# Kernel tuning notes

Measured on AMD Instinct MI355X. Metric: run time of the kernel, lower is better.

The kernel has to match this reference:

```python
import jax, jax.numpy as jnp
import numpy as np

N, K, F, E = 50000, 32, 128, 8

def setup_inputs() -> dict:
    key = jax.random.key(0)
    k1, k2, k3, k4, k5 = jax.random.split(key, 5)
    nodes = jax.random.normal(k1, (N, F), dtype=jnp.float32)
    nlist = jax.random.randint(k2, (N, K), 0, N, dtype=jnp.int64)
    edges = jax.random.normal(k3, (N, K, E), dtype=jnp.float32)
    inv_degree = jax.random.uniform(k4, (N,), dtype=jnp.float32)
    w = jax.random.normal(k5, (F, F, E), dtype=jnp.float32)
    return {"nodes": nodes, "nlist": nlist, "edges": edges,
            "inv_degree": inv_degree, "w": w}

def reference(nodes, nlist, edges, inv_degree, w):
    # gather neighbor features: [N, K, F]
    sliced = nodes[nlist]
    # 3-way contraction with neighbor-sum and inverse-degree scaling
    # edges: ijn (N,K,E); sliced: ijl (N,K,F); w: lmn (F,F,E); inv_degree: i
    out = jnp.einsum('ijn,ijl,lmn,i->im', edges, sliced, w, inv_degree)
    # activation is None (linear) per init_kwargs
    return out
```

## Files before the change

kernel.cpp:

```cpp
#include <hip/hip_runtime.h>
#include <hip/hip_bf16.h>

static constexpr int NN  = 50000;
static constexpr int KNB = 32;
static constexpr int F   = 128;
static constexpr int E   = 8;
static constexpr int TI  = 16;
static constexpr int LN  = F * E;

typedef __attribute__((ext_vector_type(8))) short short8v;
typedef __attribute__((ext_vector_type(4))) float f32x4;

__device__ __forceinline__ unsigned short f2bf(float x) {
    unsigned u = __float_as_uint(x);
    unsigned r = (u + 0x7fff + ((u >> 16) & 1)) >> 16;
    return (unsigned short)r;
}
__device__ __forceinline__ float bf2f(unsigned short b) {
    return __uint_as_float(((unsigned)b) << 16);
}

__global__ void prep_w_kernel(const float* __restrict__ w, unsigned short* __restrict__ w2f) {
    int o  = blockIdx.x * 256 + threadIdx.x;
    int e8 = o & 7, kq = (o >> 3) & 3, m = (o >> 5) & 127, kb = o >> 12;
    int k  = kb * 32 + kq * 4 + (e8 & 3) + ((e8 >> 2) << 4);
    int l  = k >> 3, n = k & 7;
    w2f[o] = f2bf(w[(size_t)(l * F + m) * E + n]);
}

__global__ void prep_nodes_kernel(const float* __restrict__ nodes, unsigned short* __restrict__ nb) {
    int t = blockIdx.x * 256 + threadIdx.x;
    const float4* s = (const float4*)nodes + (size_t)t * 2;
    float4 a = s[0], b = s[1];
    uint4 pk;
    pk.x = (unsigned)f2bf(a.x) | ((unsigned)f2bf(a.y) << 16);
    pk.y = (unsigned)f2bf(a.z) | ((unsigned)f2bf(a.w) << 16);
    pk.z = (unsigned)f2bf(b.x) | ((unsigned)f2bf(b.y) << 16);
    pk.w = (unsigned)f2bf(b.z) | ((unsigned)f2bf(b.w) << 16);
    ((uint4*)nb)[t] = pk;
}

template<bool NB>
__global__ __launch_bounds__(512, 8)
void mp_main_kernel(const float* __restrict__ nodes,
                    const unsigned short* __restrict__ nodesBf,
                    const int*   __restrict__ nlist,
                    const float* __restrict__ edges,
                    const float* __restrict__ inv_degree,
                    const unsigned short* __restrict__ w2f,
                    float* __restrict__ out)
{
    __shared__ unsigned short tS[TI * LN];
    const int tid    = threadIdx.x;
    const int wv     = __builtin_amdgcn_readfirstlane(tid >> 6);
    const int lane   = tid & 63;
    const int i_base = blockIdx.x * TI;
    char* tB = (char*)tS;

    for (int it = 0; it < 2; ++it) {
        const int row = wv * 2 + it;
        const int i   = i_base + row;
        const int*   nl = nlist + (size_t)i * KNB;
        const float* ep = edges + (size_t)i * (KNB * E);

        unsigned g[KNB];
        if (NB) {
            #pragma unroll
            for (int j = 0; j < KNB; ++j) {
                unsigned idx = (unsigned)nl[j];
                if (idx >= (unsigned)NN) idx = 0u;
                g[j] = ((const unsigned*)(nodesBf + (size_t)idx * F))[lane];
            }
        } else {
            #pragma unroll
            for (int j = 0; j < KNB; ++j) {
                unsigned idx = (unsigned)nl[j];
                if (idx >= (unsigned)NN) idx = 0u;
                const float2 fv = ((const float2*)(nodes + (size_t)idx * F))[lane];
                g[j] = ((unsigned)f2bf(fv.y) << 16) | (unsigned)f2bf(fv.x);
            }
        }
        __builtin_amdgcn_sched_barrier(0);

        float a0[E], a1[E];
        #pragma unroll
        for (int n = 0; n < E; ++n) { a0[n] = 0.f; a1[n] = 0.f; }
        #pragma unroll
        for (int j = 0; j < KNB; ++j) {
            const float v0 = bf2f((unsigned short)(g[j] & 0xffff));
            const float v1 = bf2f((unsigned short)(g[j] >> 16));
            const float4 e0 = *(const float4*)(ep + j * 8);
            const float4 e1 = *(const float4*)(ep + j * 8 + 4);
            a0[0] = __builtin_fmaf(e0.x, v0, a0[0]); a1[0] = __builtin_fmaf(e0.x, v1, a1[0]);
            a0[1] = __builtin_fmaf(e0.y, v0, a0[1]); a1[1] = __builtin_fmaf(e0.y, v1, a1[1]);
            a0[2] = __builtin_fmaf(e0.z, v0, a0[2]); a1[2] = __builtin_fmaf(e0.z, v1, a1[2]);
            a0[3] = __builtin_fmaf(e0.w, v0, a0[3]); a1[3] = __builtin_fmaf(e0.w, v1, a1[3]);
            a0[4] = __builtin_fmaf(e1.x, v0, a0[4]); a1[4] = __builtin_fmaf(e1.x, v1, a1[4]);
            a0[5] = __builtin_fmaf(e1.y, v0, a0[5]); a1[5] = __builtin_fmaf(e1.y, v1, a1[5]);
            a0[6] = __builtin_fmaf(e1.z, v0, a0[6]); a1[6] = __builtin_fmaf(e1.z, v1, a1[6]);
            a0[7] = __builtin_fmaf(e1.w, v0, a0[7]); a1[7] = __builtin_fmaf(e1.w, v1, a1[7]);
        }

        uint4 pk0, pk1;
        pk0.x = (unsigned)f2bf(a0[0]) | ((unsigned)f2bf(a0[1]) << 16);
        pk0.y = (unsigned)f2bf(a0[2]) | ((unsigned)f2bf(a0[3]) << 16);
        pk0.z = (unsigned)f2bf(a0[4]) | ((unsigned)f2bf(a0[5]) << 16);
        pk0.w = (unsigned)f2bf(a0[6]) | ((unsigned)f2bf(a0[7]) << 16);
        pk1.x = (unsigned)f2bf(a1[0]) | ((unsigned)f2bf(a1[1]) << 16);
        pk1.y = (unsigned)f2bf(a1[2]) | ((unsigned)f2bf(a1[3]) << 16);
        pk1.z = (unsigned)f2bf(a1[4]) | ((unsigned)f2bf(a1[5]) << 16);
        pk1.w = (unsigned)f2bf(a1[6]) | ((unsigned)f2bf(a1[7]) << 16);
        const int p2 = (lane >> 2) & 1;
        const int s  = (row & 7) << 4;
        const int rb = row * (LN * 2);
        const uint4 first  = p2 ? pk1 : pk0;
        const uint4 second = p2 ? pk0 : pk1;
        *(uint4*)(tB + rb + ((lane * 32 + (p2 << 4))      ^ s)) = first;
        *(uint4*)(tB + rb + ((lane * 32 + 16 - (p2 << 4)) ^ s)) = second;
    }
    __syncthreads();

    const int colm = lane & 15;
    const int kq   = lane >> 4;
    const int mt   = wv;

    f32x4 c0 = {0.f, 0.f, 0.f, 0.f};

    const int arow = colm * (LN * 2);
    const int asw  = (colm & 7) << 4;

    #pragma unroll 4
    for (int kb = 0; kb < LN / 32; ++kb) {
        union { short8v v; uint2 u[2]; } af;
        af.u[0] = *(const uint2*)(tB + arow + ((kb * 64      + kq * 8) ^ asw));
        af.u[1] = *(const uint2*)(tB + arow + ((kb * 64 + 32 + kq * 8) ^ asw));
        union { short8v v; uint4 u; } b0;
        b0.u = *(const uint4*)(w2f + ((size_t)((kb * 128 + mt * 16 + colm) * 4 + kq)) * 8);
        c0 = __builtin_amdgcn_mfma_f32_16x16x32_bf16(af.v, b0.v, c0, 0, 0, 0);
    }

    #pragma unroll
    for (int r = 0; r < 4; ++r) {
        const int ii = kq * 4 + r;
        const int gi = i_base + ii;
        out[(size_t)gi * F + mt * 16 + colm] = inv_degree[gi] * c0[r];
    }
}

__global__ __launch_bounds__(256, 2)
void mp_fused_fallback(const float* __restrict__ nodes, const int* __restrict__ nlist,
                       const float* __restrict__ edges, const float* __restrict__ inv_degree,
                       const float* __restrict__ w, float* __restrict__ out)
{
    __shared__ float tLds[TI * F * E];
    const int tid = threadIdx.x;
    const int i_base = blockIdx.x * TI;
    {
        const int l = tid & (F - 1);
        const int half = __builtin_amdgcn_readfirstlane(tid >> 7);
        for (int g = 0; g < TI / 2; ++g) {
            const int ii = g * 2 + half;
            const int i = i_base + ii;
            float acc[E];
            #pragma unroll
            for (int n = 0; n < E; ++n) acc[n] = 0.f;
            const int* nl = nlist + i * KNB;
            const float* ep = edges + (size_t)i * (KNB * E);
            #pragma unroll 4
            for (int j = 0; j < KNB; ++j) {
                unsigned idx = (unsigned)nl[j];
                if (idx >= (unsigned)NN) idx = 0u;
                const float v = nodes[idx * F + l];
                #pragma unroll
                for (int n = 0; n < E; ++n) acc[n] = __builtin_fmaf(ep[j * E + n], v, acc[n]);
            }
            float4* dst = (float4*)&tLds[ii * (F * E) + l * E];
            dst[0] = make_float4(acc[0], acc[1], acc[2], acc[3]);
            dst[1] = make_float4(acc[4], acc[5], acc[6], acc[7]);
        }
    }
    __syncthreads();
    const int m_lo = tid & 63;
    const int q = __builtin_amdgcn_readfirstlane(tid >> 6);
    float accA[TI], accB[TI];
    #pragma unroll
    for (int ii = 0; ii < TI; ++ii) { accA[ii] = 0.f; accB[ii] = 0.f; }
    for (int lq = 0; lq < F / 4; ++lq) {
        const int l = q * (F / 4) + lq;
        const float4* wp0 = (const float4*)&w[(size_t)l * (F * E) + (size_t)m_lo * E];
        const float4* wp1 = (const float4*)&w[(size_t)l * (F * E) + (size_t)(m_lo + 64) * E];
        const float4 w0a = wp0[0], w0b = wp0[1];
        const float4 w1a = wp1[0], w1b = wp1[1];
        #pragma unroll
        for (int ii = 0; ii < TI; ++ii) {
            const float4* tp = (const float4*)&tLds[ii * (F * E) + l * E];
            const float4 ta = tp[0], tb = tp[1];
            float sA = accA[ii], sB = accB[ii];
            sA = __builtin_fmaf(ta.x, w0a.x, sA); sA = __builtin_fmaf(ta.y, w0a.y, sA);
            sA = __builtin_fmaf(ta.z, w0a.z, sA); sA = __builtin_fmaf(ta.w, w0a.w, sA);
            sA = __builtin_fmaf(tb.x, w0b.x, sA); sA = __builtin_fmaf(tb.y, w0b.y, sA);
            sA = __builtin_fmaf(tb.z, w0b.z, sA); sA = __builtin_fmaf(tb.w, w0b.w, sA);
            sB = __builtin_fmaf(ta.x, w1a.x, sB); sB = __builtin_fmaf(ta.y, w1a.y, sB);
            sB = __builtin_fmaf(ta.z, w1a.z, sB); sB = __builtin_fmaf(ta.w, w1a.w, sB);
            sB = __builtin_fmaf(tb.x, w1b.x, sB); sB = __builtin_fmaf(tb.y, w1b.y, sB);
            sB = __builtin_fmaf(tb.z, w1b.z, sB); sB = __builtin_fmaf(tb.w, w1b.w, sB);
            accA[ii] = sA; accB[ii] = sB;
        }
    }
    __syncthreads();
    float* pLds = tLds;
    #pragma unroll
    for (int ii = 0; ii < TI; ++ii) {
        pLds[q * (TI * F) + ii * F + m_lo] = accA[ii];
        pLds[q * (TI * F) + ii * F + m_lo + 64] = accB[ii];
    }
    __syncthreads();
    #pragma unroll
    for (int r = 0; r < (TI * F) / 256; ++r) {
        const int o = r * 256 + tid;
        const int ii = o >> 7;
        const int m = o & (F - 1);
        const float s = pLds[0 * (TI * F) + ii * F + m] + pLds[1 * (TI * F) + ii * F + m]
                      + pLds[2 * (TI * F) + ii * F + m] + pLds[3 * (TI * F) + ii * F + m];
        const int i = i_base + ii;
        out[(size_t)i * F + m] = inv_degree[i] * s;
    }
}

extern "C" void kernel_launch(void* const* d_in, const int* in_sizes, int n_in,
                              void* d_out, int out_size, void* d_ws, size_t ws_size,
                              hipStream_t stream) {
    const float* nodes      = (const float*)d_in[0];
    const int*   nlist      = (const int*)d_in[1];
    const float* edges      = (const float*)d_in[2];
    const float* inv_degree = (const float*)d_in[3];
    const float* w          = (const float*)d_in[4];
    float* out = (float*)d_out;
    (void)in_sizes; (void)n_in; (void)out_size;

    const size_t need_w2 = (size_t)LN * F * 2;
    const size_t need_nb = (size_t)NN * F * 2;

    if (ws_size < need_w2) {
        mp_fused_fallback<<<dim3(NN / TI), dim3(256), 0, stream>>>(
            nodes, nlist, edges, inv_degree, w, out);
        return;
    }
    unsigned short* w2f = (unsigned short*)d_ws;
    unsigned short* nb  = (unsigned short*)((char*)d_ws + need_w2);

    prep_w_kernel<<<dim3((LN * F) / 256), dim3(256), 0, stream>>>(w, w2f);
    if (ws_size >= need_w2 + need_nb) {
        prep_nodes_kernel<<<dim3(NN * F / 8 / 256), dim3(256), 0, stream>>>(nodes, nb);
        mp_main_kernel<true><<<dim3(NN / TI), dim3(512), 0, stream>>>(
            nodes, nb, nlist, edges, inv_degree, w2f, out);
    } else {
        mp_main_kernel<false><<<dim3(NN / TI), dim3(512), 0, stream>>>(
            nodes, nb, nlist, edges, inv_degree, w2f, out);
    }
}
```

Baseline: 98.80 us.

## Compute neighbor-edge contraction with MFMA using double-buffered LDS staging

The first-stage contraction over neighbors (edges x gathered node features) moves from per-lane scalar FMAs to a 16x16x32 bf16 MFMA per node. Gathered features are transposed into double-buffered LDS and edges are converted to bf16 fragments, so the next node's gather overlaps the current node's MFMA. This adds 16 block-wide barriers per block, more LDS use and a lower occupancy hint. Edges are now rounded to bf16, which adds some precision loss. The fp32 fallback path is reworked to skip the bf16 round-trip on gathered values.

```diff
diff --git a/kernel.cpp b/kernel.cpp
--- a/kernel.cpp
+++ b/kernel.cpp
@@ -41,7 +41,7 @@
 }
 
 template<bool NB>
-__global__ __launch_bounds__(512, 8)
+__global__ __launch_bounds__(512, 6)
 void mp_main_kernel(const float* __restrict__ nodes,
                     const unsigned short* __restrict__ nodesBf,
                     const int*   __restrict__ nlist,
@@ -51,83 +51,122 @@
                     float* __restrict__ out)
 {
     __shared__ unsigned short tS[TI * LN];
+    __shared__ __align__(16) unsigned short ngT[2][128 * 34];
+    __shared__ __align__(16) unsigned short afS[2][512];
     const int tid    = threadIdx.x;
     const int wv     = __builtin_amdgcn_readfirstlane(tid >> 6);
     const int lane   = tid & 63;
+    const int cl     = lane & 15;
+    const int kq     = lane >> 4;
     const int i_base = blockIdx.x * TI;
     char* tB = (char*)tS;
 
-    for (int it = 0; it < 2; ++it) {
-        const int row = wv * 2 + it;
-        const int i   = i_base + row;
-        const int*   nl = nlist + (size_t)i * KNB;
-        const float* ep = edges + (size_t)i * (KNB * E);
-
-        unsigned g[KNB];
-        if (NB) {
+    if (NB) {
+        auto stage = [&](int k) {
+            const int b  = k & 1;
+            const int gi = i_base + k;
+            const int* nl = nlist + (size_t)gi * KNB;
+            unsigned pvs[4];
             #pragma unroll
-            for (int j = 0; j < KNB; ++j) {
-                unsigned idx = (unsigned)nl[j];
+            for (int jj = 0; jj < 4; ++jj) {
+                unsigned idx = (unsigned)nl[wv * 4 + jj];
                 if (idx >= (unsigned)NN) idx = 0u;
-                g[j] = ((const unsigned*)(nodesBf + (size_t)idx * F))[lane];
-            }
-        } else {
+                pvs[jj] = ((const unsigned*)(nodesBf + (size_t)idx * F))[lane];
+            }
             #pragma unroll
+            for (int jj = 0; jj < 4; ++jj) {
+                const int j = wv * 4 + jj;
+                ngT[b][(2 * lane) * 34 + j]     = (unsigned short)pvs[jj];
+                ngT[b][(2 * lane + 1) * 34 + j] = (unsigned short)(pvs[jj] >> 16);
+            }
+            if (wv == (k & 7)) {
+                unsigned fr[4] = {0u, 0u, 0u, 0u};
+                #pragma unroll
+                for (int e = 0; e < 8; ++e) {
+                    const int j = kq * 4 + (e & 3) + ((e >> 2) << 4);
+                    float v = 0.f;
+                    if (cl < 8) v = edges[(size_t)gi * (KNB * E) + j * E + cl];
+                    fr[e >> 1] |= (unsigned)f2bf(v) << ((e & 1) * 16);
+                }
+                *(uint4*)(&afS[b][lane * 8]) = make_uint4(fr[0], fr[1], fr[2], fr[3]);
+            }
+        };
+        auto compute = [&](int k) {
+            const int b = k & 1;
+            union { short8v v; uint4 u; } ea;
+            ea.u = *(const uint4*)(&afS[b][lane * 8]);
+            const char* ngB = (const char*)&ngT[b][0];
+            const int rowb = (wv * 16 + cl) * 68;
+            union { short8v v; unsigned u[4]; } bb;
+            bb.u[0] = *(const unsigned*)(ngB + rowb + kq * 8);
+            bb.u[1] = *(const unsigned*)(ngB + rowb + kq * 8 + 4);
+            bb.u[2] = *(const unsigned*)(ngB + rowb + 32 + kq * 8);
+            bb.u[3] = *(const unsigned*)(ngB + rowb + 32 + kq * 8 + 4);
+            f32x4 d = {0.f, 0.f, 0.f, 0.f};
+            d = __builtin_amdgcn_mfma_f32_16x16x32_bf16(ea.v, bb.v, d, 0, 0, 0);
+            if (kq < 2) {
+                const unsigned d0 = (unsigned)f2bf(d[0]) | ((unsigned)f2bf(d[1]) << 16);
+                const unsigned d1 = (unsigned)f2bf(d[2]) | ((unsigned)f2bf(d[3]) << 16);
+                const int lg = wv * 16 + cl;
+                const int bp = lg * 16 + kq * 8;
+                *(uint2*)(tB + k * (LN * 2) + (bp ^ ((k & 7) << 4))) = make_uint2(d0, d1);
+            }
+        };
+        stage(0);
+        __syncthreads();
+        for (int k = 0; k < TI; ++k) {
+            if (k < TI - 1) stage(k + 1);
+            compute(k);
+            __syncthreads();
+        }
+    } else {
+        for (int it = 0; it < 2; ++it) {
+            const int row = wv * 2 + it;
+            const int i   = i_base + row;
+            const int*   nl = nlist + (size_t)i * KNB;
+            const float* ep = edges + (size_t)i * (KNB * E);
+            float a0[E], a1[E];
+            #pragma unroll
+            for (int n = 0; n < E; ++n) { a0[n] = 0.f; a1[n] = 0.f; }
+            #pragma unroll 4
             for (int j = 0; j < KNB; ++j) {
                 unsigned idx = (unsigned)nl[j];
                 if (idx >= (unsigned)NN) idx = 0u;
                 const float2 fv = ((const float2*)(nodes + (size_t)idx * F))[lane];
-                g[j] = ((unsigned)f2bf(fv.y) << 16) | (unsigned)f2bf(fv.x);
-            }
+                const float4 e0 = *(const float4*)(ep + j * 8);
+                const float4 e1 = *(const float4*)(ep + j * 8 + 4);
+                a0[0] = __builtin_fmaf(e0.x, fv.x, a0[0]); a1[0] = __builtin_fmaf(e0.x, fv.y, a1[0]);
+                a0[1] = __builtin_fmaf(e0.y, fv.x, a0[1]); a1[1] = __builtin_fmaf(e0.y, fv.y, a1[1]);
+                a0[2] = __builtin_fmaf(e0.z, fv.x, a0[2]); a1[2] = __builtin_fmaf(e0.z, fv.y, a1[2]);
+                a0[3] = __builtin_fmaf(e0.w, fv.x, a0[3]); a1[3] = __builtin_fmaf(e0.w, fv.y, a1[3]);
+                a0[4] = __builtin_fmaf(e1.x, fv.x, a0[4]); a1[4] = __builtin_fmaf(e1.x, fv.y, a1[4]);
+                a0[5] = __builtin_fmaf(e1.y, fv.x, a0[5]); a1[5] = __builtin_fmaf(e1.y, fv.y, a1[5]);
+                a0[6] = __builtin_fmaf(e1.z, fv.x, a0[6]); a1[6] = __builtin_fmaf(e1.z, fv.y, a1[6]);
+                a0[7] = __builtin_fmaf(e1.w, fv.x, a0[7]); a1[7] = __builtin_fmaf(e1.w, fv.y, a1[7]);
+            }
+            uint4 pk0, pk1;
+            pk0.x = (unsigned)f2bf(a0[0]) | ((unsigned)f2bf(a0[1]) << 16);
+            pk0.y = (unsigned)f2bf(a0[2]) | ((unsigned)f2bf(a0[3]) << 16);
+            pk0.z = (unsigned)f2bf(a0[4]) | ((unsigned)f2bf(a0[5]) << 16);
+            pk0.w = (unsigned)f2bf(a0[6]) | ((unsigned)f2bf(a0[7]) << 16);
+            pk1.x = (unsigned)f2bf(a1[0]) | ((unsigned)f2bf(a1[1]) << 16);
+            pk1.y = (unsigned)f2bf(a1[2]) | ((unsigned)f2bf(a1[3]) << 16);
+            pk1.z = (unsigned)f2bf(a1[4]) | ((unsigned)f2bf(a1[5]) << 16);
+            pk1.w = (unsigned)f2bf(a1[6]) | ((unsigned)f2bf(a1[7]) << 16);
+            const int s  = (row & 7) << 4;
+            const int rb = row * (LN * 2);
+            *(uint4*)(tB + rb + ((lane * 32)      ^ s)) = pk0;
+            *(uint4*)(tB + rb + ((lane * 32 + 16) ^ s)) = pk1;
         }
-        __builtin_amdgcn_sched_barrier(0);
-
-        float a0[E], a1[E];
-        #pragma unroll
-        for (int n = 0; n < E; ++n) { a0[n] = 0.f; a1[n] = 0.f; }
-        #pragma unroll
-        for (int j = 0; j < KNB; ++j) {
-            const float v0 = bf2f((unsigned short)(g[j] & 0xffff));
-            const float v1 = bf2f((unsigned short)(g[j] >> 16));
-            const float4 e0 = *(const float4*)(ep + j * 8);
-            const float4 e1 = *(const float4*)(ep + j * 8 + 4);
-            a0[0] = __builtin_fmaf(e0.x, v0, a0[0]); a1[0] = __builtin_fmaf(e0.x, v1, a1[0]);
-            a0[1] = __builtin_fmaf(e0.y, v0, a0[1]); a1[1] = __builtin_fmaf(e0.y, v1, a1[1]);
-            a0[2] = __builtin_fmaf(e0.z, v0, a0[2]); a1[2] = __builtin_fmaf(e0.z, v1, a1[2]);
-            a0[3] = __builtin_fmaf(e0.w, v0, a0[3]); a1[3] = __builtin_fmaf(e0.w, v1, a1[3]);
-            a0[4] = __builtin_fmaf(e1.x, v0, a0[4]); a1[4] = __builtin_fmaf(e1.x, v1, a1[4]);
-            a0[5] = __builtin_fmaf(e1.y, v0, a0[5]); a1[5] = __builtin_fmaf(e1.y, v1, a1[5]);
-            a0[6] = __builtin_fmaf(e1.z, v0, a0[6]); a1[6] = __builtin_fmaf(e1.z, v1, a1[6]);
-            a0[7] = __builtin_fmaf(e1.w, v0, a0[7]); a1[7] = __builtin_fmaf(e1.w, v1, a1[7]);
-        }
-
-        uint4 pk0, pk1;
-        pk0.x = (unsigned)f2bf(a0[0]) | ((unsigned)f2bf(a0[1]) << 16);
-        pk0.y = (unsigned)f2bf(a0[2]) | ((unsigned)f2bf(a0[3]) << 16);
-        pk0.z = (unsigned)f2bf(a0[4]) | ((unsigned)f2bf(a0[5]) << 16);
-        pk0.w = (unsigned)f2bf(a0[6]) | ((unsigned)f2bf(a0[7]) << 16);
-        pk1.x = (unsigned)f2bf(a1[0]) | ((unsigned)f2bf(a1[1]) << 16);
-        pk1.y = (unsigned)f2bf(a1[2]) | ((unsigned)f2bf(a1[3]) << 16);
-        pk1.z = (unsigned)f2bf(a1[4]) | ((unsigned)f2bf(a1[5]) << 16);
-        pk1.w = (unsigned)f2bf(a1[6]) | ((unsigned)f2bf(a1[7]) << 16);
-        const int p2 = (lane >> 2) & 1;
-        const int s  = (row & 7) << 4;
-        const int rb = row * (LN * 2);
-        const uint4 first  = p2 ? pk1 : pk0;
-        const uint4 second = p2 ? pk0 : pk1;
-        *(uint4*)(tB + rb + ((lane * 32 + (p2 << 4))      ^ s)) = first;
-        *(uint4*)(tB + rb + ((lane * 32 + 16 - (p2 << 4)) ^ s)) = second;
-    }
-    __syncthreads();
-
-    const int colm = lane & 15;
-    const int kq   = lane >> 4;
-    const int mt   = wv;
+        __syncthreads();
+    }
+
+    const int mt = wv;
 
     f32x4 c0 = {0.f, 0.f, 0.f, 0.f};
 
-    const int arow = colm * (LN * 2);
-    const int asw  = (colm & 7) << 4;
+    const int arow = cl * (LN * 2);
+    const int asw  = (cl & 7) << 4;
 
     #pragma unroll 4
     for (int kb = 0; kb < LN / 32; ++kb) {
@@ -135,7 +174,7 @@
         af.u[0] = *(const uint2*)(tB + arow + ((kb * 64      + kq * 8) ^ asw));
         af.u[1] = *(const uint2*)(tB + arow + ((kb * 64 + 32 + kq * 8) ^ asw));
         union { short8v v; uint4 u; } b0;
-        b0.u = *(const uint4*)(w2f + ((size_t)((kb * 128 + mt * 16 + colm) * 4 + kq)) * 8);
+        b0.u = *(const uint4*)(w2f + ((size_t)((kb * 128 + mt * 16 + cl) * 4 + kq)) * 8);
         c0 = __builtin_amdgcn_mfma_f32_16x16x32_bf16(af.v, b0.v, c0, 0, 0, 0);
     }
 
@@ -143,7 +182,7 @@
     for (int r = 0; r < 4; ++r) {
         const int ii = kq * 4 + r;
         const int gi = i_base + ii;
-        out[(size_t)gi * F + mt * 16 + colm] = inv_degree[gi] * c0[r];
+        out[(size_t)gi * F + mt * 16 + cl] = inv_degree[gi] * c0[r];
     }
 }
 
```

After: 147.9 us. 1.5x slower.

## Use packed FP32 FMAs with scalar edge operands and hardware bf16 pack in gather stage

Applied to the files above, without the earlier changes.

The gather-contract stage is rewritten to interleave each neighbor's gather with its FMAs instead of first issuing all 32 gathers into registers. Neighbor indices are made wave-uniform with readfirstlane, and edge weights are passed as scalar operands to v_pk_fma_f32, halving the VALU FMA count. The final float-to-bf16 rounding uses v_cvt_pk_bf16_f32 instead of software rounding. The trade-off is less memory-level parallelism, since the batched gather and sched_barrier are gone. There is also a risk that the "s" constraint on per-row float2 edge values forces extra scalar moves or fails to compile.

```diff
diff --git a/kernel.cpp b/kernel.cpp
--- a/kernel.cpp
+++ b/kernel.cpp
@@ -15,9 +15,6 @@
     unsigned u = __float_as_uint(x);
     unsigned r = (u + 0x7fff + ((u >> 16) & 1)) >> 16;
     return (unsigned short)r;
-}
-__device__ __forceinline__ float bf2f(unsigned short b) {
-    return __uint_as_float(((unsigned)b) << 16);
 }
 
 __global__ void prep_w_kernel(const float* __restrict__ w, unsigned short* __restrict__ w2f) {
@@ -63,53 +60,49 @@
         const int*   nl = nlist + (size_t)i * KNB;
         const float* ep = edges + (size_t)i * (KNB * E);
 
-        unsigned g[KNB];
-        if (NB) {
-            #pragma unroll
-            for (int j = 0; j < KNB; ++j) {
-                unsigned idx = (unsigned)nl[j];
-                if (idx >= (unsigned)NN) idx = 0u;
-                g[j] = ((const unsigned*)(nodesBf + (size_t)idx * F))[lane];
-            }
-        } else {
-            #pragma unroll
-            for (int j = 0; j < KNB; ++j) {
-                unsigned idx = (unsigned)nl[j];
-                if (idx >= (unsigned)NN) idx = 0u;
-                const float2 fv = ((const float2*)(nodes + (size_t)idx * F))[lane];
-                g[j] = ((unsigned)f2bf(fv.y) << 16) | (unsigned)f2bf(fv.x);
-            }
-        }
-        __builtin_amdgcn_sched_barrier(0);
-
-        float a0[E], a1[E];
+        float2 p0[4], p1[4];
         #pragma unroll
-        for (int n = 0; n < E; ++n) { a0[n] = 0.f; a1[n] = 0.f; }
+        for (int q = 0; q < 4; ++q) { p0[q] = make_float2(0.f, 0.f); p1[q] = make_float2(0.f, 0.f); }
+
         #pragma unroll
         for (int j = 0; j < KNB; ++j) {
-            const float v0 = bf2f((unsigned short)(g[j] & 0xffff));
-            const float v1 = bf2f((unsigned short)(g[j] >> 16));
-            const float4 e0 = *(const float4*)(ep + j * 8);
-            const float4 e1 = *(const float4*)(ep + j * 8 + 4);
-            a0[0] = __builtin_fmaf(e0.x, v0, a0[0]); a1[0] = __builtin_fmaf(e0.x, v1, a1[0]);
-            a0[1] = __builtin_fmaf(e0.y, v0, a0[1]); a1[1] = __builtin_fmaf(e0.y, v1, a1[1]);
-            a0[2] = __builtin_fmaf(e0.z, v0, a0[2]); a1[2] = __builtin_fmaf(e0.z, v1, a1[2]);
-            a0[3] = __builtin_fmaf(e0.w, v0, a0[3]); a1[3] = __builtin_fmaf(e0.w, v1, a1[3]);
-            a0[4] = __builtin_fmaf(e1.x, v0, a0[4]); a1[4] = __builtin_fmaf(e1.x, v1, a1[4]);
-            a0[5] = __builtin_fmaf(e1.y, v0, a0[5]); a1[5] = __builtin_fmaf(e1.y, v1, a1[5]);
-            a0[6] = __builtin_fmaf(e1.z, v0, a0[6]); a1[6] = __builtin_fmaf(e1.z, v1, a1[6]);
-            a0[7] = __builtin_fmaf(e1.w, v0, a0[7]); a1[7] = __builtin_fmaf(e1.w, v1, a1[7]);
+            unsigned idx = (unsigned)nl[j];
+            if (idx >= (unsigned)NN) idx = 0u;
+            idx = __builtin_amdgcn_readfirstlane(idx);
+            unsigned g;
+            if (NB) {
+                g = ((const unsigned*)(nodesBf + (size_t)idx * F))[lane];
+            } else {
+                const float2 fv = ((const float2*)(nodes + (size_t)idx * F))[lane];
+                g = ((unsigned)f2bf(fv.y) << 16) | (unsigned)f2bf(fv.x);
+            }
+            const float2 e01 = *(const float2*)(ep + j * 8 + 0);
+            const float2 e23 = *(const float2*)(ep + j * 8 + 2);
+            const float2 e45 = *(const float2*)(ep + j * 8 + 4);
+            const float2 e67 = *(const float2*)(ep + j * 8 + 6);
+            float2 vv0, vv1;
+            vv0.x = __uint_as_float(g << 16);         vv0.y = vv0.x;
+            vv1.x = __uint_as_float(g & 0xffff0000u); vv1.y = vv1.x;
+            asm("v_pk_fma_f32 %0, %1, %2, %0" : "+v"(p0[0]) : "s"(e01), "v"(vv0));
+            asm("v_pk_fma_f32 %0, %1, %2, %0" : "+v"(p0[1]) : "s"(e23), "v"(vv0));
+            asm("v_pk_fma_f32 %0, %1, %2, %0" : "+v"(p0[2]) : "s"(e45), "v"(vv0));
+            asm("v_pk_fma_f32 %0, %1, %2, %0" : "+v"(p0[3]) : "s"(e67), "v"(vv0));
+            asm("v_pk_fma_f32 %0, %1, %2, %0" : "+v"(p1[0]) : "s"(e01), "v"(vv1));
+            asm("v_pk_fma_f32 %0, %1, %2, %0" : "+v"(p1[1]) : "s"(e23), "v"(vv1));
+            asm("v_pk_fma_f32 %0, %1, %2, %0" : "+v"(p1[2]) : "s"(e45), "v"(vv1));
+            asm("v_pk_fma_f32 %0, %1, %2, %0" : "+v"(p1[3]) : "s"(e67), "v"(vv1));
         }
 
         uint4 pk0, pk1;
-        pk0.x = (unsigned)f2bf(a0[0]) | ((unsigned)f2bf(a0[1]) << 16);
-        pk0.y = (unsigned)f2bf(a0[2]) | ((unsigned)f2bf(a0[3]) << 16);
-        pk0.z = (unsigned)f2bf(a0[4]) | ((unsigned)f2bf(a0[5]) << 16);
-        pk0.w = (unsigned)f2bf(a0[6]) | ((unsigned)f2bf(a0[7]) << 16);
-        pk1.x = (unsigned)f2bf(a1[0]) | ((unsigned)f2bf(a1[1]) << 16);
-        pk1.y = (unsigned)f2bf(a1[2]) | ((unsigned)f2bf(a1[3]) << 16);
-        pk1.z = (unsigned)f2bf(a1[4]) | ((unsigned)f2bf(a1[5]) << 16);
-        pk1.w = (unsigned)f2bf(a1[6]) | ((unsigned)f2bf(a1[7]) << 16);
+        asm("v_cvt_pk_bf16_f32 %0, %1, %2" : "=v"(pk0.x) : "v"(p0[0].x), "v"(p0[0].y));
+        asm("v_cvt_pk_bf16_f32 %0, %1, %2" : "=v"(pk0.y) : "v"(p0[1].x), "v"(p0[1].y));
+        asm("v_cvt_pk_bf16_f32 %0, %1, %2" : "=v"(pk0.z) : "v"(p0[2].x), "v"(p0[2].y));
+        asm("v_cvt_pk_bf16_f32 %0, %1, %2" : "=v"(pk0.w) : "v"(p0[3].x), "v"(p0[3].y));
+        asm("v_cvt_pk_bf16_f32 %0, %1, %2" : "=v"(pk1.x) : "v"(p1[0].x), "v"(p1[0].y));
+        asm("v_cvt_pk_bf16_f32 %0, %1, %2" : "=v"(pk1.y) : "v"(p1[1].x), "v"(p1[1].y));
+        asm("v_cvt_pk_bf16_f32 %0, %1, %2" : "=v"(pk1.z) : "v"(p1[2].x), "v"(p1[2].y));
+        asm("v_cvt_pk_bf16_f32 %0, %1, %2" : "=v"(pk1.w) : "v"(p1[3].x), "v"(p1[3].y));
+
         const int p2 = (lane >> 2) & 1;
         const int s  = (row & 7) << 4;
         const int rb = row * (LN * 2);
```

Result: slower. 101.3 us (+2.6%).

## Stream neighbor gathers into LDS via async global_load_lds with double buffering

Applied to the files above, without the earlier changes.

Replaces the register-held gather of all 32 neighbor rows with asynchronous global-to-LDS loads in chunks of four neighbors, double-buffered per wave with explicit vmcnt waits so gathers overlap the FMA accumulation. Also switches bf16 packing to the hardware v_cvt_pk_bf16_f32 instruction and lowers the occupancy hint to 6. This cuts register pressure from the 32-entry gather array but adds LDS usage and relies on hand-written waitcnt ordering. The fallback path now triggers whenever the bf16 node workspace is unavailable. An unused prefetch-depth-2 variant is left in.

```diff
diff --git a/kernel.cpp b/kernel.cpp
--- a/kernel.cpp
+++ b/kernel.cpp
@@ -16,8 +16,13 @@
     unsigned r = (u + 0x7fff + ((u >> 16) & 1)) >> 16;
     return (unsigned short)r;
 }
-__device__ __forceinline__ float bf2f(unsigned short b) {
-    return __uint_as_float(((unsigned)b) << 16);
+__device__ __forceinline__ float bf2f_lo(unsigned g) { return __uint_as_float(g << 16); }
+__device__ __forceinline__ float bf2f_hi(unsigned g) { return __uint_as_float(g & 0xffff0000u); }
+
+__device__ __forceinline__ void gload_lds4(const unsigned* gsrc, unsigned* ldst) {
+    __builtin_amdgcn_global_load_lds(
+        (const __attribute__((address_space(1))) unsigned*)gsrc,
+        (__attribute__((address_space(3))) unsigned*)ldst, 4, 0, 0);
 }
 
 __global__ void prep_w_kernel(const float* __restrict__ w, unsigned short* __restrict__ w2f) {
@@ -40,10 +45,8 @@
     ((uint4*)nb)[t] = pk;
 }
 
-template<bool NB>
-__global__ __launch_bounds__(512, 8)
-void mp_main_kernel(const float* __restrict__ nodes,
-                    const unsigned short* __restrict__ nodesBf,
+__global__ __launch_bounds__(512, 6)
+void mp_main_kernel(const unsigned short* __restrict__ nodesBf,
                     const int*   __restrict__ nlist,
                     const float* __restrict__ edges,
                     const float* __restrict__ inv_degree,
@@ -51,72 +54,81 @@
                     float* __restrict__ out)
 {
     __shared__ unsigned short tS[TI * LN];
+    __shared__ unsigned stgW[8][2][4 * 64];
     const int tid    = threadIdx.x;
     const int wv     = __builtin_amdgcn_readfirstlane(tid >> 6);
     const int lane   = tid & 63;
     const int i_base = blockIdx.x * TI;
     char* tB = (char*)tS;
 
-    for (int it = 0; it < 2; ++it) {
-        const int row = wv * 2 + it;
-        const int i   = i_base + row;
-        const int*   nl = nlist + (size_t)i * KNB;
-        const float* ep = edges + (size_t)i * (KNB * E);
-
-        unsigned g[KNB];
-        if (NB) {
-            #pragma unroll
-            for (int j = 0; j < KNB; ++j) {
-                unsigned idx = (unsigned)nl[j];
+    {
+        const int i0 = i_base + wv * 2;
+        const int*   nl = nlist + (size_t)i0 * KNB;
+        const float* ep = edges + (size_t)i0 * (KNB * E);
+
+        auto issue = [&](int c) {
+            const int* nlr = nl + c * 4;
+            unsigned* dst = &stgW[wv][c & 1][0];
+            #pragma unroll
+            for (int q = 0; q < 4; ++q) {
+                unsigned idx = (unsigned)nlr[q];
                 if (idx >= (unsigned)NN) idx = 0u;
-                g[j] = ((const unsigned*)(nodesBf + (size_t)idx * F))[lane];
-            }
-        } else {
-            #pragma unroll
-            for (int j = 0; j < KNB; ++j) {
-                unsigned idx = (unsigned)nl[j];
-                if (idx >= (unsigned)NN) idx = 0u;
-                const float2 fv = ((const float2*)(nodes + (size_t)idx * F))[lane];
-                g[j] = ((unsigned)f2bf(fv.y) << 16) | (unsigned)f2bf(fv.x);
-            }
+                gload_lds4((const unsigned*)(nodesBf + (size_t)idx * F) + lane, dst + q * 64);
+            }
+        };
+
+        float a0[E], a1[E];
+        #pragma unroll
+        for (int n = 0; n < E; ++n) { a0[n] = 0.f; a1[n] = 0.f; }
+
+        auto store_row = [&](int row) {
+            uint4 pk0, pk1;
+            asm("v_cvt_pk_bf16_f32 %0, %1, %2" : "=v"(pk0.x) : "v"(a0[0]), "v"(a0[1]));
+            asm("v_cvt_pk_bf16_f32 %0, %1, %2" : "=v"(pk0.y) : "v"(a0[2]), "v"(a0[3]));
+            asm("v_cvt_pk_bf16_f32 %0, %1, %2" : "=v"(pk0.z) : "v"(a0[4]), "v"(a0[5]));
+            asm("v_cvt_pk_bf16_f32 %0, %1, %2" : "=v"(pk0.w) : "v"(a0[6]), "v"(a0[7]));
+            asm("v_cvt_pk_bf16_f32 %0, %1, %2" : "=v"(pk1.x) : "v"(a1[0]), "v"(a1[1]));
+            asm("v_cvt_pk_bf16_f32 %0, %1, %2" : "=v"(pk1.y) : "v"(a1[2]), "v"(a1[3]));
+            asm("v_cvt_pk_bf16_f32 %0, %1, %2" : "=v"(pk1.z) : "v"(a1[4]), "v"(a1[5]));
+            asm("v_cvt_pk_bf16_f32 %0, %1, %2" : "=v"(pk1.w) : "v"(a1[6]), "v"(a1[7]));
+            const int p2 = (lane >> 2) & 1;
+            const int s  = (row & 7) << 4;
+            const int rb = row * (LN * 2);
+            const uint4 first  = p2 ? pk1 : pk0;
+            const uint4 second = p2 ? pk0 : pk1;
+            *(uint4*)(tB + rb + ((lane * 32 + (p2 << 4))      ^ s)) = first;
+            *(uint4*)(tB + rb + ((lane * 32 + 16 - (p2 << 4)) ^ s)) = second;
+            #pragma unroll
+            for (int n = 0; n < E; ++n) { a0[n] = 0.f; a1[n] = 0.f; }
+        };
+
+        issue(0);
+        issue(1);
+        #pragma unroll
+        for (int c = 0; c < 16; ++c) {
+            if (c + 2 < 16) issue(c + 2);
+            if (c < 15) { asm volatile("s_waitcnt vmcnt(8)" ::: "memory"); }
+            else        { asm volatile("s_waitcnt vmcnt(0)" ::: "memory"); }
+            const unsigned* sb = &stgW[wv][c & 1][0];
+            const float* epc = ep + (c * 4) * E;
+            #pragma unroll
+            for (int q = 0; q < 4; ++q) {
+                const unsigned g = sb[q * 64 + lane];
+                const float v0 = bf2f_lo(g), v1 = bf2f_hi(g);
+                const float4 e0 = *(const float4*)(epc + q * 8);
+                const float4 e1 = *(const float4*)(epc + q * 8 + 4);
+                a0[0] = __builtin_fmaf(e0.x, v0, a0[0]); a1[0] = __builtin_fmaf(e0.x, v1, a1[0]);
+                a0[1] = __builtin_fmaf(e0.y, v0, a0[1]); a1[1] = __builtin_fmaf(e0.y, v1, a1[1]);
+                a0[2] = __builtin_fmaf(e0.z, v0, a0[2]); a1[2] = __builtin_fmaf(e0.z, v1, a1[2]);
+                a0[3] = __builtin_fmaf(e0.w, v0, a0[3]); a1[3] = __builtin_fmaf(e0.w, v1, a1[3]);
+                a0[4] = __builtin_fmaf(e1.x, v0, a0[4]); a1[4] = __builtin_fmaf(e1.x, v1, a1[4]);
+                a0[5] = __builtin_fmaf(e1.y, v0, a0[5]); a1[5] = __builtin_fmaf(e1.y, v1, a1[5]);
+                a0[6] = __builtin_fmaf(e1.z, v0, a0[6]); a1[6] = __builtin_fmaf(e1.z, v1, a1[6]);
+                a0[7] = __builtin_fmaf(e1.w, v0, a0[7]); a1[7] = __builtin_fmaf(e1.w, v1, a1[7]);
+            }
+            if (c == 7)  store_row(wv * 2);
+            if (c == 15) store_row(wv * 2 + 1);
         }
-        __builtin_amdgcn_sched_barrier(0);
-
-        float a0[E], a1[E];
-        #pragma unroll
-        for (int n = 0; n < E; ++n) { a0[n] = 0.f; a1[n] = 0.f; }
-        #pragma unroll
-        for (int j = 0; j < KNB; ++j) {
-            const float v0 = bf2f((unsigned short)(g[j] & 0xffff));
-            const float v1 = bf2f((unsigned short)(g[j] >> 16));
-            const float4 e0 = *(const float4*)(ep + j * 8);
-            const float4 e1 = *(const float4*)(ep + j * 8 + 4);
-            a0[0] = __builtin_fmaf(e0.x, v0, a0[0]); a1[0] = __builtin_fmaf(e0.x, v1, a1[0]);
-            a0[1] = __builtin_fmaf(e0.y, v0, a0[1]); a1[1] = __builtin_fmaf(e0.y, v1, a1[1]);
-            a0[2] = __builtin_fmaf(e0.z, v0, a0[2]); a1[2] = __builtin_fmaf(e0.z, v1, a1[2]);
-            a0[3] = __builtin_fmaf(e0.w, v0, a0[3]); a1[3] = __builtin_fmaf(e0.w, v1, a1[3]);
-            a0[4] = __builtin_fmaf(e1.x, v0, a0[4]); a1[4] = __builtin_fmaf(e1.x, v1, a1[4]);
-            a0[5] = __builtin_fmaf(e1.y, v0, a0[5]); a1[5] = __builtin_fmaf(e1.y, v1, a1[5]);
-            a0[6] = __builtin_fmaf(e1.z, v0, a0[6]); a1[6] = __builtin_fmaf(e1.z, v1, a1[6]);
-            a0[7] = __builtin_fmaf(e1.w, v0, a0[7]); a1[7] = __builtin_fmaf(e1.w, v1, a1[7]);
-        }
-
-        uint4 pk0, pk1;
-        pk0.x = (unsigned)f2bf(a0[0]) | ((unsigned)f2bf(a0[1]) << 16);
-        pk0.y = (unsigned)f2bf(a0[2]) | ((unsigned)f2bf(a0[3]) << 16);
-        pk0.z = (unsigned)f2bf(a0[4]) | ((unsigned)f2bf(a0[5]) << 16);
-        pk0.w = (unsigned)f2bf(a0[6]) | ((unsigned)f2bf(a0[7]) << 16);
-        pk1.x = (unsigned)f2bf(a1[0]) | ((unsigned)f2bf(a1[1]) << 16);
-        pk1.y = (unsigned)f2bf(a1[2]) | ((unsigned)f2bf(a1[3]) << 16);
-        pk1.z = (unsigned)f2bf(a1[4]) | ((unsigned)f2bf(a1[5]) << 16);
-        pk1.w = (unsigned)f2bf(a1[6]) | ((unsigned)f2bf(a1[7]) << 16);
-        const int p2 = (lane >> 2) & 1;
-        const int s  = (row & 7) << 4;
-        const int rb = row * (LN * 2);
-        const uint4 first  = p2 ? pk1 : pk0;
-        const uint4 second = p2 ? pk0 : pk1;
-        *(uint4*)(tB + rb + ((lane * 32 + (p2 << 4))      ^ s)) = first;
-        *(uint4*)(tB + rb + ((lane * 32 + 16 - (p2 << 4)) ^ s)) = second;
     }
     __syncthreads();
 
@@ -126,6 +138,121 @@
 
     f32x4 c0 = {0.f, 0.f, 0.f, 0.f};
 
+    const int arow = colm * (LN * 2);
+    const int asw  = (colm & 7) << 4;
+
+    #pragma unroll 4
+    for (int kb = 0; kb < LN / 32; ++kb) {
+        union { short8v v; uint2 u[2]; } af;
+        af.u[0] = *(const uint2*)(tB + arow + ((kb * 64      + kq * 8) ^ asw));
+        af.u[1] = *(const uint2*)(tB + arow + ((kb * 64 + 32 + kq * 8) ^ asw));
+        union { short8v v; uint4 u; } b0;
+        b0.u = *(const uint4*)(w2f + ((size_t)((kb * 128 + mt * 16 + colm) * 4 + kq)) * 8);
+        c0 = __builtin_amdgcn_mfma_f32_16x16x32_bf16(af.v, b0.v, c0, 0, 0, 0);
+    }
+
+    #pragma unroll
+    for (int r = 0; r < 4; ++r) {
+        const int ii = kq * 4 + r;
+        const int gi = i_base + ii;
+        out[(size_t)gi * F + mt * 16 + colm] = inv_degree[gi] * c0[r];
+    }
+}
+
+__global__ __launch_bounds__(512, 6)
+void mp_main_kernel2(const unsigned short* __restrict__ nodesBf,
+                     const int*   __restrict__ nlist,
+                     const float* __restrict__ edges,
+                     const float* __restrict__ inv_degree,
+                     const unsigned short* __restrict__ w2f,
+                     float* __restrict__ out)
+{
+    __shared__ unsigned short tS[TI * LN];
+    __shared__ unsigned stgW[8][2][4 * 64];
+    const int tid    = threadIdx.x;
+    const int wv     = __builtin_amdgcn_readfirstlane(tid >> 6);
+    const int lane   = tid & 63;
+    const int i_base = blockIdx.x * TI;
+    char* tB = (char*)tS;
+
+    {
+        const int i0 = i_base + wv * 2;
+        const int*   nl = nlist + (size_t)i0 * KNB;
+        const float* ep = edges + (size_t)i0 * (KNB * E);
+
+        auto issue = [&](int c) {
+            const int* nlr = nl + c * 4;
+            unsigned* dst = &stgW[wv][c & 1][0];
+            #pragma unroll
+            for (int q = 0; q < 4; ++q) {
+                unsigned idx = (unsigned)nlr[q];
+                if (idx >= (unsigned)NN) idx = 0u;
+                gload_lds4((const unsigned*)(nodesBf + (size_t)idx * F) + lane, dst + q * 64);
+            }
+        };
+
+        float a0[E], a1[E];
+        #pragma unroll
+        for (int n = 0; n < E; ++n) { a0[n] = 0.f; a1[n] = 0.f; }
+
+        auto store_row = [&](int row) {
+            uint4 pk0, pk1;
+            asm("v_cvt_pk_bf16_f32 %0, %1, %2" : "=v"(pk0.x) : "v"(a0[0]), "v"(a0[1]));
+            asm("v_cvt_pk_bf16_f32 %0, %1, %2" : "=v"(pk0.y) : "v"(a0[2]), "v"(a0[3]));
+            asm("v_cvt_pk_bf16_f32 %0, %1, %2" : "=v"(pk0.z) : "v"(a0[4]), "v"(a0[5]));
+            asm("v_cvt_pk_bf16_f32 %0, %1, %2" : "=v"(pk0.w) : "v"(a0[6]), "v"(a0[7]));
+            asm("v_cvt_pk_bf16_f32 %0, %1, %2" : "=v"(pk1.x) : "v"(a1[0]), "v"(a1[1]));
+            asm("v_cvt_pk_bf16_f32 %0, %1, %2" : "=v"(pk1.y) : "v"(a1[2]), "v"(a1[3]));
+            asm("v_cvt_pk_bf16_f32 %0, %1, %2" : "=v"(pk1.z) : "v"(a1[4]), "v"(a1[5]));
+            asm("v_cvt_pk_bf16_f32 %0, %1, %2" : "=v"(pk1.w) : "v"(a1[6]), "v"(a1[7]));
+            const int p2 = (lane >> 2) & 1;
+            const int s  = (row & 7) << 4;
+            const int rb = row * (LN * 2);
+            const uint4 first  = p2 ? pk1 : pk0;
+            const uint4 second = p2 ? pk0 : pk1;
+            *(uint4*)(tB + rb + ((lane * 32 + (p2 << 4))      ^ s)) = first;
+            *(uint4*)(tB + rb + ((lane * 32 + 16 - (p2 << 4)) ^ s)) = second;
+            #pragma unroll
+            for (int n = 0; n < E; ++n) { a0[n] = 0.f; a1[n] = 0.f; }
+        };
+
+        issue(0);
+        #pragma unroll
+        for (int c = 0; c < 16; ++c) {
+            if (c + 1 < 16) {
+                issue(c + 1);
+                asm volatile("s_waitcnt vmcnt(4)" ::: "memory");
+            } else {
+                asm volatile("s_waitcnt vmcnt(0)" ::: "memory");
+            }
+            const unsigned* sb = &stgW[wv][c & 1][0];
+            const float* epc = ep + (c * 4) * E;
+            #pragma unroll
+            for (int q = 0; q < 4; ++q) {
+                const unsigned g = sb[q * 64 + lane];
+                const float v0 = bf2f_lo(g), v1 = bf2f_hi(g);
+                const float4 e0 = *(const float4*)(epc + q * 8);
+                const float4 e1 = *(const float4*)(epc + q * 8 + 4);
+                a0[0] = __builtin_fmaf(e0.x, v0, a0[0]); a1[0] = __builtin_fmaf(e0.x, v1, a1[0]);
+                a0[1] = __builtin_fmaf(e0.y, v0, a0[1]); a1[1] = __builtin_fmaf(e0.y, v1, a1[1]);
+                a0[2] = __builtin_fmaf(e0.z, v0, a0[2]); a1[2] = __builtin_fmaf(e0.z, v1, a1[2]);
+                a0[3] = __builtin_fmaf(e0.w, v0, a0[3]); a1[3] = __builtin_fmaf(e0.w, v1, a1[3]);
+                a0[4] = __builtin_fmaf(e1.x, v0, a0[4]); a1[4] = __builtin_fmaf(e1.x, v1, a1[4]);
+                a0[5] = __builtin_fmaf(e1.y, v0, a0[5]); a1[5] = __builtin_fmaf(e1.y, v1, a1[5]);
+                a0[6] = __builtin_fmaf(e1.z, v0, a0[6]); a1[6] = __builtin_fmaf(e1.z, v1, a1[6]);
+                a0[7] = __builtin_fmaf(e1.w, v0, a0[7]); a1[7] = __builtin_fmaf(e1.w, v1, a1[7]);
+            }
+            if (c == 7)  store_row(wv * 2);
+            if (c == 15) store_row(wv * 2 + 1);
+        }
+    }
+    __syncthreads();
+
+    const int colm = lane & 15;
+    const int kq   = lane >> 4;
+    const int mt   = wv;
+
+    f32x4 c0 = {0.f, 0.f, 0.f, 0.f};
     const int arow = colm * (LN * 2);
     const int asw  = (colm & 7) << 4;
 
@@ -241,7 +368,7 @@
     const size_t need_w2 = (size_t)LN * F * 2;
     const size_t need_nb = (size_t)NN * F * 2;
 
-    if (ws_size < need_w2) {
+    if (ws_size < need_w2 + need_nb) {
         mp_fused_fallback<<<dim3(NN / TI), dim3(256), 0, stream>>>(
             nodes, nlist, edges, inv_degree, w, out);
         return;
@@ -250,12 +377,7 @@
     unsigned short* nb  = (unsigned short*)((char*)d_ws + need_w2);
 
     prep_w_kernel<<<dim3((LN * F) / 256), dim3(256), 0, stream>>>(w, w2f);
-    if (ws_size >= need_w2 + need_nb) {
-        prep_nodes_kernel<<<dim3(NN * F / 8 / 256), dim3(256), 0, stream>>>(nodes, nb);
-        mp_main_kernel<true><<<dim3(NN / TI), dim3(512), 0, stream>>>(
-            nodes, nb, nlist, edges, inv_degree, w2f, out);
-    } else {
-        mp_main_kernel<false><<<dim3(NN / TI), dim3(512), 0, stream>>>(
-            nodes, nb, nlist, edges, inv_degree, w2f, out);
-    }
-}
+    prep_nodes_kernel<<<dim3(NN * F / 8 / 256), dim3(256), 0, stream>>>(nodes, nb);
+    mp_main_kernel2<<<dim3(NN / TI), dim3(512), 0, stream>>>(
+        nb, nlist, edges, inv_degree, w2f, out);
+}
```

Result: slower. 113.7 us (+15.1%).
